# Kernel tuning notes

Hardware: AMD Instinct MI355X
Metric: run time of the kernel (lower is better)

Reference implementation:

```python
import jax, jax.numpy as jnp
import numpy as np

N, C_IN, C_OUT, K_CHEB, BATCH = 2048, 64, 64, 4, 8


def setup_inputs() -> dict:
    key = jax.random.key(0)
    k1, k2, k3, k4, k5 = jax.random.split(key, 5)
    # Xavier-uniform-like scales
    s_nn = float(np.sqrt(6.0 / (N + N)))
    s_th = float(np.sqrt(6.0 / (C_IN + C_OUT)))
    return {
        "X": jax.random.normal(k1, (BATCH, N, C_IN), dtype=jnp.float32),
        "Ws": jax.random.uniform(k2, (N, N), jnp.float32, -s_nn, s_nn),
        "W_alpha": jax.random.uniform(k3, (N, N), jnp.float32, -s_nn, s_nn),
        "Theta_s": jax.random.uniform(k4, (K_CHEB, C_IN, C_OUT), jnp.float32, -s_th, s_th),
        "Theta_d": jax.random.uniform(k5, (K_CHEB, C_IN, C_OUT), jnp.float32, -s_th, s_th),
    }


def reference(X, Ws, W_alpha, Theta_s, Theta_d):
    B, n, c_in = X.shape
    K = Theta_s.shape[0]

    # ---- static filter: sum_k (T_k(Ws) @ X) @ Theta_s[k] ----
    # T_0 = I, so T_0 @ X = X
    static_filter = jnp.einsum('bni,io->bno', X, Theta_s[0])
    if K > 1:
        T_prev2 = jnp.eye(n, dtype=X.dtype)
        T_prev1 = Ws  # T_1
        for k in range(1, K):
            TkX = jnp.einsum('nm,bmi->bni', T_prev1, X)
            static_filter = static_filter + jnp.einsum('bni,io->bno', TkX, Theta_s[k])
            if k + 1 < K:  # incremental Chebyshev recursion (same values as from-scratch)
                T_prev2, T_prev1 = T_prev1, 2.0 * (Ws @ T_prev1) - T_prev2

    # ---- dynamic filter ----
    # Wd = X @ (W_alpha @ X)^T  -> [B, n, n]
    WaX = jnp.einsum('nm,bmi->bni', W_alpha, X)
    Wd = jnp.einsum('bni,bmi->bnm', X, WaX)

    dynamic_filter = jnp.einsum('bni,io->bno', X, Theta_d[0])
    if K > 1:
        Td_prev2 = jnp.broadcast_to(jnp.eye(n, dtype=X.dtype), (B, n, n))
        Td_prev1 = Wd  # T_1
        for k in range(1, K):
            TkX = jnp.einsum('bnm,bmi->bni', Td_prev1, X)
            dynamic_filter = dynamic_filter + jnp.einsum('bni,io->bno', TkX, Theta_d[k])
            if k + 1 < K:
                Td_prev2, Td_prev1 = Td_prev1, 2.0 * jnp.matmul(Wd, Td_prev1) - Td_prev2

    return jax.nn.relu(static_filter) + jax.nn.relu(dynamic_filter)
```

## Files before the change

kernel.cpp:

```cpp
#include <hip/hip_runtime.h>

typedef __attribute__((ext_vector_type(8))) short bf16x8;
typedef __attribute__((ext_vector_type(4))) float f32x4;

__device__ __forceinline__ ushort f32_to_bf16(float f) {
    union { float f; unsigned u; } v; v.f = f;
    unsigned b = v.u + 0x7FFF + ((v.u >> 16) & 1);
    return (ushort)(b >> 16);
}
__device__ __forceinline__ float bf16_to_f32(ushort h) {
    union { unsigned u; float f; } v; v.u = ((unsigned)h) << 16;
    return v.f;
}
__device__ __forceinline__ void split2(float x, ushort& a, ushort& b) {
    a = f32_to_bf16(x); float r1 = x - bf16_to_f32(a);
    b = f32_to_bf16(r1);
}

__device__ __forceinline__ void vmwait8() { asm volatile("s_waitcnt vmcnt(8)" ::: "memory"); }
__device__ __forceinline__ void vmwait0() { asm volatile("s_waitcnt vmcnt(0)" ::: "memory"); }
__device__ __forceinline__ void lgwait0() { asm volatile("s_waitcnt lgkmcnt(0)" ::: "memory"); }
__device__ __forceinline__ void blockbar() {
    __builtin_amdgcn_sched_barrier(0);
    __builtin_amdgcn_s_barrier();
    __builtin_amdgcn_sched_barrier(0);
}

__device__ __forceinline__ void stage64x64(const ushort* gsrc, int row_stride_elems,
                                           char* lds, int t256) {
    const char* gb = (const char*)gsrc;
    const int rs = row_stride_elems * 2;
#pragma unroll
    for (int j = 0; j < 2; ++j) {
        int o = (j * 256 + t256) * 16;
        int row = o >> 7;
        int col = (o & 127) ^ ((row & 7) << 4);
        __builtin_amdgcn_global_load_lds(
            (const __attribute__((address_space(1))) unsigned int*)(gb + row * rs + col),
            (__attribute__((address_space(3))) unsigned int*)(lds + o), 16, 0, 0);
    }
}
__device__ __forceinline__ bf16x8 fragld(const char* lds, int row, int kbyte) {
    return *(const bf16x8*)(lds + (row << 7) + (kbyte ^ ((row & 7) << 4)));
}

__device__ __forceinline__ void stage64x128(const ushort* gsrc, char* lds, int t) {
    const char* gb = (const char*)gsrc;
#pragma unroll
    for (int j = 0; j < 4; ++j) {
        int o = (j * 256 + t) * 16;
        int row = o >> 8;
        int col = (o & 255) ^ ((row & 7) << 4);
        __builtin_amdgcn_global_load_lds(
            (const __attribute__((address_space(1))) unsigned int*)(gb + row * 4096 + col),
            (__attribute__((address_space(3))) unsigned int*)(lds + o), 16, 0, 0);
    }
}
__device__ __forceinline__ bf16x8 fragld256(const char* lds, int row, int kbyte) {
    return *(const bf16x8*)(lds + (row << 8) + (kbyte ^ ((row & 7) << 4)));
}

__global__ __launch_bounds__(256) void prep_all(const float* __restrict__ X,
        ushort* __restrict__ XT1, ushort* __restrict__ XT2,
        ushort* __restrict__ X1o, ushort* __restrict__ X2o,
        const float* __restrict__ Ws, ushort* __restrict__ Ws16,
        const float* __restrict__ Wa, ushort* __restrict__ Wa1,
        const float* __restrict__ Ths, ushort* __restrict__ ThsT) {
    __shared__ float tile[64][68];
    const int bx = blockIdx.x;
    const int t = threadIdx.x;
    if (bx < 256) {
        const int b = bx >> 5, n0 = (bx & 31) * 64;
#pragma unroll
        for (int it = 0; it < 4; ++it) {
            int f = it * 256 + t, r = f >> 4, q = (f & 15) * 4;
            float4 v = *(const float4*)&X[((size_t)b * 2048 + n0 + r) * 64 + q];
            tile[r][q + 0] = v.x; tile[r][q + 1] = v.y; tile[r][q + 2] = v.z; tile[r][q + 3] = v.w;
        }
        __syncthreads();
#pragma unroll
        for (int it = 0; it < 4; ++it) {
            int f = it * 256 + t, c = f >> 4, q = (f & 15) * 4;
            ushort4 h1, h2;
            split2(tile[q + 0][c], h1.x, h2.x); split2(tile[q + 1][c], h1.y, h2.y);
            split2(tile[q + 2][c], h1.z, h2.z); split2(tile[q + 3][c], h1.w, h2.w);
            size_t a = (size_t)(b * 64 + c) * 2048 + n0 + q;
            *(ushort4*)&XT1[a] = h1; *(ushort4*)&XT2[a] = h2;
        }
#pragma unroll
        for (int it = 0; it < 4; ++it) {
            int f = it * 256 + t, n = f >> 4, q = (f & 15) * 4;
            ushort4 h1, h2;
            split2(tile[n][q + 0], h1.x, h2.x); split2(tile[n][q + 1], h1.y, h2.y);
            split2(tile[n][q + 2], h1.z, h2.z); split2(tile[n][q + 3], h1.w, h2.w);
            size_t a = (size_t)(n0 + n) * 512 + b * 64 + q;
            *(ushort4*)&X1o[a] = h1; *(ushort4*)&X2o[a] = h2;
        }
    } else if (bx < 2304) {
        size_t idx = ((size_t)(bx - 256) * 256 + t) * 8;
#pragma unroll
        for (int h = 0; h < 2; ++h) {
            float4 v = *(const float4*)&Ws[idx + h * 4];
            ushort4 a;
            a.x = f32_to_bf16(v.x); a.y = f32_to_bf16(v.y);
            a.z = f32_to_bf16(v.z); a.w = f32_to_bf16(v.w);
            *(ushort4*)&Ws16[idx + h * 4] = a;
        }
    } else if (bx < 4352) {
        size_t idx = ((size_t)(bx - 2304) * 256 + t) * 8;
#pragma unroll
        for (int h = 0; h < 2; ++h) {
            float4 v = *(const float4*)&Wa[idx + h * 4];
            ushort4 a;
            a.x = f32_to_bf16(v.x); a.y = f32_to_bf16(v.y);
            a.z = f32_to_bf16(v.z); a.w = f32_to_bf16(v.w);
            *(ushort4*)&Wa1[idx + h * 4] = a;
        }
    } else {
        int idx = (bx - 4352) * 256 + t;
        int k = idx >> 12, o = (idx >> 6) & 63, i = idx & 63;
        ThsT[idx] = f32_to_bf16(Ths[k * 4096 + i * 64 + o]);
    }
}

template <int MODE>
__device__ __forceinline__ void gemm_sv2(int bx, const ushort* __restrict__ A,
        const ushort* __restrict__ BT, const ushort* __restrict__ CinT,
        ushort* __restrict__ YT, ushort* __restrict__ Yo, char* ls) {
    const int t = threadIdx.x;
    const int m0 = (bx & 31) * 64, c0 = (bx >> 5) * 64;
    const int w = t >> 6, lane = t & 63, l15 = lane & 15, l4 = lane >> 4;
    const int kb = w * 64 + l4 * 16;
    const ushort* Ap = A + (size_t)m0 * 2048;
    const ushort* Bp = BT + (size_t)c0 * 2048;

    f32x4 z = {0.f, 0.f, 0.f, 0.f};
    f32x4 acc[4][4];
#pragma unroll
    for (int i = 0; i < 4; ++i)
#pragma unroll
        for (int j = 0; j < 4; ++j) acc[i][j] = z;

    stage64x128(Ap, ls, t);
    stage64x128(Bp, ls + 16384, t);
    for (int ts = 0; ts < 16; ++ts) {
        char* cur = ls + (ts & 1) * 32768;
        if (ts < 15) {
            char* nxt = ls + ((ts + 1) & 1) * 32768;
            stage64x128(Ap + (ts + 1) * 128, nxt, t);
            stage64x128(Bp + (ts + 1) * 128, nxt + 16384, t);
            vmwait8();
        } else {
            vmwait0();
        }
        blockbar();
        bf16x8 aF[4], bF[4];
#pragma unroll
        for (int i = 0; i < 4; ++i) aF[i] = fragld256(cur, i * 16 + l15, kb);
#pragma unroll
        for (int j = 0; j < 4; ++j) bF[j] = fragld256(cur + 16384, j * 16 + l15, kb);
#pragma unroll
        for (int i = 0; i < 4; ++i)
#pragma unroll
            for (int j = 0; j < 4; ++j)
                acc[i][j] = __builtin_amdgcn_mfma_f32_16x16x32_bf16(aF[i], bF[j], acc[i][j], 0, 0, 0);
        lgwait0();
        blockbar();
    }

    float* red = (float*)ls;
    ushort* tileo = (ushort*)(ls + 50176);
    if (w < 3) {
#pragma unroll
        for (int i = 0; i < 4; ++i)
#pragma unroll
            for (int j = 0; j < 4; ++j) {
                const int row = i * 16 + l4 * 4;
                const int col = j * 16 + l15;
#pragma unroll
                for (int r = 0; r < 4; ++r) red[w * 4160 + (row + r) * 65 + col] = acc[i][j][r];
            }
    }
    __syncthreads();
    if (w == 3) {
#pragma unroll
        for (int i = 0; i < 4; ++i)
#pragma unroll
            for (int j = 0; j < 4; ++j) {
                const int row = i * 16 + l4 * 4;
                const int col = j * 16 + l15;
                float vv[4];
#pragma unroll
                for (int r = 0; r < 4; ++r) {
                    const int rr = (row + r) * 65 + col;
                    vv[r] = acc[i][j][r] + red[rr] + red[4160 + rr] + red[8320 + rr];
                }
                if (MODE == 1) {
                    ushort4 ci = *(const ushort4*)&CinT[(size_t)(c0 + col) * 2048 + m0 + row];
                    vv[0] = 2.f * vv[0] - bf16_to_f32(ci.x);
                    vv[1] = 2.f * vv[1] - bf16_to_f32(ci.y);
                    vv[2] = 2.f * vv[2] - bf16_to_f32(ci.z);
                    vv[3] = 2.f * vv[3] - bf16_to_f32(ci.w);
                }
                ushort4 p;
                p.x = f32_to_bf16(vv[0]); p.y = f32_to_bf16(vv[1]);
                p.z = f32_to_bf16(vv[2]); p.w = f32_to_bf16(vv[3]);
                *(ushort4*)&YT[(size_t)(c0 + col) * 2048 + m0 + row] = p;
                tileo[(row + 0) * 64 + col] = p.x;
                tileo[(row + 1) * 64 + col] = p.y;
                tileo[(row + 2) * 64 + col] = p.z;
                tileo[(row + 3) * 64 + col] = p.w;
            }
    }
    __syncthreads();
#pragma unroll
    for (int it = 0; it < 2; ++it) {
        int f = it * 256 + t;
        int row = f >> 3, ch = f & 7;
        *(uint4*)&Yo[(size_t)(m0 + row) * 512 + c0 + ch * 8] = *(uint4*)&tileo[row * 64 + ch * 8];
    }
}

__device__ __forceinline__ void gemm3v2(int bx, const ushort* __restrict__ A1,
        const ushort* __restrict__ B1, const ushort* __restrict__ B2,
        float* __restrict__ WaXT, char* ls) {
    const int t = threadIdx.x;
    const int m0 = (bx & 31) * 64, c0 = (bx >> 5) * 64;
    const int w = t >> 6, lane = t & 63, l15 = lane & 15, l4 = lane >> 4;
    const int kb = w * 64 + l4 * 16;

    f32x4 z = {0.f, 0.f, 0.f, 0.f};
    f32x4 acc[4][4];
#pragma unroll
    for (int i = 0; i < 4; ++i)
#pragma unroll
        for (int j = 0; j < 4; ++j) acc[i][j] = z;

    for (int k0 = 0; k0 < 2048; k0 += 128) {
        stage64x128(A1 + (size_t)m0 * 2048 + k0, ls, t);
        stage64x128(B1 + (size_t)c0 * 2048 + k0, ls + 16384, t);
        stage64x128(B2 + (size_t)c0 * 2048 + k0, ls + 32768, t);
        __syncthreads();
        bf16x8 aF[4], b1F[4], b2F[4];
#pragma unroll
        for (int i = 0; i < 4; ++i) {
            aF[i]  = fragld256(ls, i * 16 + l15, kb);
            b1F[i] = fragld256(ls + 16384, i * 16 + l15, kb);
            b2F[i] = fragld256(ls + 32768, i * 16 + l15, kb);
        }
#pragma unroll
        for (int i = 0; i < 4; ++i)
#pragma unroll
            for (int j = 0; j < 4; ++j) {
                f32x4 a = acc[i][j];
                a = __builtin_amdgcn_mfma_f32_16x16x32_bf16(aF[i], b1F[j], a, 0, 0, 0);
                a = __builtin_amdgcn_mfma_f32_16x16x32_bf16(aF[i], b2F[j], a, 0, 0, 0);
                acc[i][j] = a;
            }
        __syncthreads();
    }

    float* red = (float*)ls;
    if (w < 3) {
#pragma unroll
        for (int i = 0; i < 4; ++i)
#pragma unroll
            for (int j = 0; j < 4; ++j) {
                const int row = i * 16 + l4 * 4;
                const int col = j * 16 + l15;
#pragma unroll
                for (int r = 0; r < 4; ++r) red[w * 4160 + (row + r) * 65 + col] = acc[i][j][r];
            }
    }
    __syncthreads();
    if (w == 3) {
#pragma unroll
        for (int i = 0; i < 4; ++i)
#pragma unroll
            for (int j = 0; j < 4; ++j) {
                const int row = i * 16 + l4 * 4;
                const int col = j * 16 + l15;
                f32x4 v;
#pragma unroll
                for (int r = 0; r < 4; ++r) {
                    const int rr = (row + r) * 65 + col;
                    v[r] = acc[i][j][r] + red[rr] + red[4160 + rr] + red[8320 + rr];
                }
                *(f32x4*)&WaXT[(size_t)(c0 + col) * 2048 + m0 + row] = v;
            }
    }
}

__device__ __forceinline__ void gramv2(int bx, const float* __restrict__ WaXT,
        const ushort* __restrict__ XT1, const ushort* __restrict__ XT2,
        float* __restrict__ Gpart, char* lsraw) {
    const int b = bx & 7, chunk = bx >> 3;
    float (*Lw)[68] = (float(*)[68])lsraw;
    float (*Rx)[68] = (float(*)[68])(lsraw + 17408);
    const int t = threadIdx.x;
    const int n0 = chunk * 64;
    {
        const int r = t >> 2, q = (t & 3) * 16;
        size_t a = (size_t)(b * 64 + r) * 2048 + n0 + q;
#pragma unroll
        for (int h = 0; h < 4; ++h) {
            *(float4*)&Lw[r][q + h * 4] = *(const float4*)&WaXT[a + h * 4];
            ushort4 h1 = *(const ushort4*)&XT1[a + h * 4];
            ushort4 h2 = *(const ushort4*)&XT2[a + h * 4];
            Rx[r][q + h * 4 + 0] = bf16_to_f32(h1.x) + bf16_to_f32(h2.x);
            Rx[r][q + h * 4 + 1] = bf16_to_f32(h1.y) + bf16_to_f32(h2.y);
            Rx[r][q + h * 4 + 2] = bf16_to_f32(h1.z) + bf16_to_f32(h2.z);
            Rx[r][q + h * 4 + 3] = bf16_to_f32(h1.w) + bf16_to_f32(h2.w);
        }
    }
    __syncthreads();
    {
        const int tx = t & 15, ty = t >> 4;
        float acc[4][4] = {{0.f,0.f,0.f,0.f},{0.f,0.f,0.f,0.f},{0.f,0.f,0.f,0.f},{0.f,0.f,0.f,0.f}};
        for (int n = 0; n < 64; ++n) {
            float a[4], bb[4];
#pragma unroll
            for (int i = 0; i < 4; ++i) { a[i] = Lw[ty * 4 + i][n]; bb[i] = Rx[tx * 4 + i][n]; }
#pragma unroll
            for (int i = 0; i < 4; ++i)
#pragma unroll
                for (int j = 0; j < 4; ++j) acc[i][j] = fmaf(a[i], bb[j], acc[i][j]);
        }
        float* gp = Gpart + (size_t)(chunk * 8 + b) * 4096;
#pragma unroll
        for (int i = 0; i < 4; ++i)
            *(float4*)&gp[(ty * 4 + i) * 64 + tx * 4] =
                make_float4(acc[i][0], acc[i][1], acc[i][2], acc[i][3]);
    }
}

__device__ __forceinline__ void chebv2(int b, const float* __restrict__ Gpart,
        const float* __restrict__ Thd, ushort* __restrict__ DT1, ushort* __restrict__ DT2,
        char* lsraw) {
    float (*Gs)[68]  = (float(*)[68])lsraw;
    float (*C2s)[68] = (float(*)[68])(lsraw + 17408);
    float (*C3s)[68] = (float(*)[68])(lsraw + 34816);
    const int t = threadIdx.x;
    for (int i = t; i < 4096; i += 256) {
        float s = 0.f;
#pragma unroll
        for (int c = 0; c < 32; ++c) s += Gpart[((size_t)c * 8 + b) * 4096 + i];
        Gs[i >> 6][i & 63] = s;
    }
    __syncthreads();
    const int tx = t & 15, ty = t >> 4;
    const int r0 = ty * 4, c0 = tx * 4;

    {
        float p[4][4] = {{0,0,0,0},{0,0,0,0},{0,0,0,0},{0,0,0,0}};
        for (int k = 0; k < 64; ++k) {
            float ar[4] = {Gs[r0][k], Gs[r0+1][k], Gs[r0+2][k], Gs[r0+3][k]};
            float4 bv = *(const float4*)&Gs[k][c0];
            float br[4] = {bv.x, bv.y, bv.z, bv.w};
#pragma unroll
            for (int i = 0; i < 4; ++i)
#pragma unroll
                for (int j = 0; j < 4; ++j) p[i][j] = fmaf(ar[i], br[j], p[i][j]);
        }
#pragma unroll
        for (int i = 0; i < 4; ++i)
#pragma unroll
            for (int j = 0; j < 4; ++j)
                C2s[r0+i][c0+j] = 2.f * p[i][j] - ((r0+i) == (c0+j) ? 1.f : 0.f);
    }
    __syncthreads();
    {
        float q[4][4] = {{0,0,0,0},{0,0,0,0},{0,0,0,0},{0,0,0,0}};
        for (int k = 0; k < 64; ++k) {
            float ar[4] = {Gs[r0][k], Gs[r0+1][k], Gs[r0+2][k], Gs[r0+3][k]};
            float4 bv = *(const float4*)&C2s[k][c0];
            float br[4] = {bv.x, bv.y, bv.z, bv.w};
#pragma unroll
            for (int i = 0; i < 4; ++i)
#pragma unroll
                for (int j = 0; j < 4; ++j) q[i][j] = fmaf(ar[i], br[j], q[i][j]);
        }
#pragma unroll
        for (int i = 0; i < 4; ++i)
#pragma unroll
            for (int j = 0; j < 4; ++j)
                C3s[r0+i][c0+j] = 2.f * q[i][j] - Gs[r0+i][c0+j];
    }
    __syncthreads();
    float d[4][4];
    {
#pragma unroll
        for (int i = 0; i < 4; ++i) {
            float4 t0 = *(const float4*)&Thd[(r0+i) * 64 + c0];
            d[i][0] = t0.x; d[i][1] = t0.y; d[i][2] = t0.z; d[i][3] = t0.w;
        }
        for (int k = 0; k < 64; ++k) {
            float4 t1 = *(const float4*)&Thd[4096 + k * 64 + c0];
            float4 t2 = *(const float4*)&Thd[8192 + k * 64 + c0];
            float4 t3 = *(const float4*)&Thd[12288 + k * 64 + c0];
            float a1[4] = {Gs[r0][k], Gs[r0+1][k], Gs[r0+2][k], Gs[r0+3][k]};
            float a2[4] = {C2s[r0][k], C2s[r0+1][k], C2s[r0+2][k], C2s[r0+3][k]};
            float a3[4] = {C3s[r0][k], C3s[r0+1][k], C3s[r0+2][k], C3s[r0+3][k]};
            float b1[4] = {t1.x, t1.y, t1.z, t1.w};
            float b2[4] = {t2.x, t2.y, t2.z, t2.w};
            float b3[4] = {t3.x, t3.y, t3.z, t3.w};
#pragma unroll
            for (int i = 0; i < 4; ++i)
#pragma unroll
                for (int j = 0; j < 4; ++j) {
                    d[i][j] = fmaf(a1[i], b1[j], d[i][j]);
                    d[i][j] = fmaf(a2[i], b2[j], d[i][j]);
                    d[i][j] = fmaf(a3[i], b3[j], d[i][j]);
                }
        }
    }
    __syncthreads();
#pragma unroll
    for (int i = 0; i < 4; ++i)
#pragma unroll
        for (int j = 0; j < 4; ++j) Gs[r0 + i][c0 + j] = d[i][j];
    __syncthreads();
#pragma unroll
    for (int it = 0; it < 16; ++it) {
        int idx = it * 256 + t;
        int o = idx >> 6, ii = idx & 63;
        ushort h1, h2;
        split2(Gs[ii][o], h1, h2);
        DT1[b * 4096 + idx] = h1;
        DT2[b * 4096 + idx] = h2;
    }
}

__global__ __launch_bounds__(256, 2) void mega1(const ushort* __restrict__ Wa1,
        const ushort* __restrict__ XT1, const ushort* __restrict__ XT2,
        float* __restrict__ WaXT,
        const ushort* __restrict__ Ws16, ushort* __restrict__ Y1T, ushort* __restrict__ Y1o) {
    __shared__ __align__(16) char ls[65536];
    const int bx = blockIdx.x;
    if (bx < 256) gemm3v2(bx, Wa1, XT1, XT2, WaXT, ls);
    else          gemm_sv2<0>(bx - 256, Ws16, XT1, nullptr, Y1T, Y1o, ls);
}

__global__ __launch_bounds__(256, 2) void mega2(const ushort* __restrict__ Ws16,
        const ushort* __restrict__ Y1T, const ushort* __restrict__ XT1,
        ushort* __restrict__ Y2T, ushort* __restrict__ Y2o,
        const float* __restrict__ WaXT, const ushort* __restrict__ XT2,
        float* __restrict__ Gpart) {
    __shared__ __align__(16) char ls[65536];
    const int bx = blockIdx.x;
    if (bx < 256) gemm_sv2<1>(bx, Ws16, Y1T, XT1, Y2T, Y2o, ls);
    else          gramv2(bx - 256, WaXT, XT1, XT2, Gpart, ls);
}

__global__ __launch_bounds__(256, 2) void mega3(const ushort* __restrict__ Ws16,
        const ushort* __restrict__ Y2T, const ushort* __restrict__ Y1T,
        ushort* __restrict__ Y3T, ushort* __restrict__ Y3o,
        const float* __restrict__ Gpart, const float* __restrict__ Thd,
        ushort* __restrict__ DT1, ushort* __restrict__ DT2) {
    __shared__ __align__(16) char ls[65536];
    const int bx = blockIdx.x;
    if (bx < 256) gemm_sv2<1>(bx, Ws16, Y2T, Y1T, Y3T, Y3o, ls);
    else          chebv2(bx - 256, Gpart, Thd, DT1, DT2, ls);
}

__global__ __launch_bounds__(256) void ep_fused(const ushort* __restrict__ ThsT,
                                                const ushort* __restrict__ DT1, const ushort* __restrict__ DT2,
                                                const ushort* __restrict__ X1o, const ushort* __restrict__ X2o,
                                                const ushort* __restrict__ Y1o, const ushort* __restrict__ Y2o,
                                                const ushort* __restrict__ Y3o,
                                                float* __restrict__ out) {
    __shared__ __align__(16) char ls[65536];
    const int b = blockIdx.y, n0 = blockIdx.x * 64;
    const int t = threadIdx.x, lane = t & 63, w = t >> 6, wr = w >> 1, wc = w & 1;
    const int l15 = lane & 15, l4 = lane >> 4;
    stage64x64(X1o + (size_t)n0 * 512 + b * 64, 512, ls + 0 * 8192, t);
    stage64x64(Y1o + (size_t)n0 * 512 + b * 64, 512, ls + 1 * 8192, t);
    stage64x64(Y2o + (size_t)n0 * 512 + b * 64, 512, ls + 2 * 8192, t);
    stage64x64(Y3o + (size_t)n0 * 512 + b * 64, 512, ls + 3 * 8192, t);
    stage64x64(ThsT + 0 * 4096, 64, ls + 4 * 8192, t);
    stage64x64(ThsT + 1 * 4096, 64, ls + 5 * 8192, t);
    stage64x64(ThsT + 2 * 4096, 64, ls + 6 * 8192, t);
    stage64x64(ThsT + 3 * 4096, 64, ls + 7 * 8192, t);
    __syncthreads();
    f32x4 z = {0.f, 0.f, 0.f, 0.f};
    f32x4 as[2][2], ad[2][2];
    as[0][0] = z; as[0][1] = z; as[1][0] = z; as[1][1] = z;
    ad[0][0] = z; ad[0][1] = z; ad[1][0] = z; ad[1][1] = z;
#pragma unroll
    for (int s = 0; s < 2; ++s) {
        const int kb = s * 64 + l4 * 16;
#pragma unroll
        for (int p = 0; p < 4; ++p) {
            bf16x8 aF[2], bF[2];
#pragma unroll
            for (int f = 0; f < 2; ++f) {
                aF[f] = fragld(ls + (4 + p) * 8192, wr * 32 + f * 16 + l15, kb);
                bF[f] = fragld(ls + p * 8192, wc * 32 + f * 16 + l15, kb);
            }
#pragma unroll
            for (int i = 0; i < 2; ++i)
#pragma unroll
                for (int j = 0; j < 2; ++j)
                    as[i][j] = __builtin_amdgcn_mfma_f32_16x16x32_bf16(aF[i], bF[j], as[i][j], 0, 0, 0);
        }
    }
    __syncthreads();
    stage64x64(DT1 + b * 4096, 64, ls + 1 * 8192, t);
    stage64x64(DT2 + b * 4096, 64, ls + 2 * 8192, t);
    stage64x64(X2o + (size_t)n0 * 512 + b * 64, 512, ls + 3 * 8192, t);
    __syncthreads();
#pragma unroll
    for (int s = 0; s < 2; ++s) {
        const int kb = s * 64 + l4 * 16;
        bf16x8 a1[2], a2[2], b0[2], b3[2];
#pragma unroll
        for (int f = 0; f < 2; ++f) {
            a1[f] = fragld(ls + 1 * 8192, wr * 32 + f * 16 + l15, kb);
            a2[f] = fragld(ls + 2 * 8192, wr * 32 + f * 16 + l15, kb);
            b0[f] = fragld(ls + 0 * 8192, wc * 32 + f * 16 + l15, kb);
            b3[f] = fragld(ls + 3 * 8192, wc * 32 + f * 16 + l15, kb);
        }
#pragma unroll
        for (int i = 0; i < 2; ++i)
#pragma unroll
            for (int j = 0; j < 2; ++j) {
                f32x4 a = ad[i][j];
                a = __builtin_amdgcn_mfma_f32_16x16x32_bf16(a1[i], b0[j], a, 0, 0, 0);
                a = __builtin_amdgcn_mfma_f32_16x16x32_bf16(a1[i], b3[j], a, 0, 0, 0);
                a = __builtin_amdgcn_mfma_f32_16x16x32_bf16(a2[i], b0[j], a, 0, 0, 0);
                ad[i][j] = a;
            }
    }
#pragma unroll
    for (int i = 0; i < 2; ++i)
#pragma unroll
        for (int j = 0; j < 2; ++j) {
            const int ob = wr * 32 + i * 16 + l4 * 4;
            const int nn = wc * 32 + j * 16 + l15;
            float4 o4;
            o4.x = fmaxf(as[i][j][0], 0.f) + fmaxf(ad[i][j][0], 0.f);
            o4.y = fmaxf(as[i][j][1], 0.f) + fmaxf(ad[i][j][1], 0.f);
            o4.z = fmaxf(as[i][j][2], 0.f) + fmaxf(ad[i][j][2], 0.f);
            o4.w = fmaxf(as[i][j][3], 0.f) + fmaxf(ad[i][j][3], 0.f);
            *(float4*)&out[((size_t)b * 2048 + n0 + nn) * 64 + ob] = o4;
        }
}

extern "C" void kernel_launch(void* const* d_in, const int* in_sizes, int n_in,
                              void* d_out, int out_size, void* d_ws, size_t ws_size,
                              hipStream_t stream) {
    (void)in_sizes; (void)n_in; (void)out_size;
    const float* X   = (const float*)d_in[0];
    const float* Ws  = (const float*)d_in[1];
    const float* Wa  = (const float*)d_in[2];
    const float* Ths = (const float*)d_in[3];
    const float* Thd = (const float*)d_in[4];

    char* p = (char*)d_ws;
    auto alloc = [&](size_t bytes) { char* r = p; p += (bytes + 255) & ~(size_t)255; return r; };
    ushort* XT1 = (ushort*)alloc(512ull * 2048 * 2);
    ushort* XT2 = (ushort*)alloc(512ull * 2048 * 2);
    ushort* X1o = (ushort*)alloc(2048ull * 512 * 2);
    ushort* X2o = (ushort*)alloc(2048ull * 512 * 2);
    ushort* Ws16 = (ushort*)alloc(2048ull * 2048 * 2);
    ushort* Wa1 = (ushort*)alloc(2048ull * 2048 * 2);
    ushort* Y1T = (ushort*)alloc(512ull * 2048 * 2);
    ushort* Y2T = (ushort*)alloc(512ull * 2048 * 2);
    ushort* Y3T = (ushort*)alloc(512ull * 2048 * 2);
    ushort* Y1o = (ushort*)alloc(2048ull * 512 * 2);
    ushort* Y2o = (ushort*)alloc(2048ull * 512 * 2);
    ushort* Y3o = (ushort*)alloc(2048ull * 512 * 2);
    float*  Gpart = (float*)alloc(32ull * 8 * 4096 * 4);
    ushort* DT1 = (ushort*)alloc(8ull * 4096 * 2);
    ushort* DT2 = (ushort*)alloc(8ull * 4096 * 2);
    ushort* ThsT = (ushort*)alloc(4ull * 4096 * 2);
    if ((size_t)(p - (char*)d_ws) > ws_size) return;
    float* WaXT = (float*)d_out;

    prep_all<<<4416, 256, 0, stream>>>(X, XT1, XT2, X1o, X2o, Ws, Ws16, Wa, Wa1, Ths, ThsT);
    mega1<<<512, 256, 0, stream>>>(Wa1, XT1, XT2, WaXT, Ws16, Y1T, Y1o);
    mega2<<<512, 256, 0, stream>>>(Ws16, Y1T, XT1, Y2T, Y2o, WaXT, XT2, Gpart);
    mega3<<<264, 256, 0, stream>>>(Ws16, Y2T, Y1T, Y3T, Y3o, Gpart, Thd, DT1, DT2);
    ep_fused<<<dim3(32, 8), 256, 0, stream>>>(ThsT, DT1, DT2, X1o, X2o, Y1o, Y2o, Y3o, (float*)d_out);
}
```

Before: 87.85 us.

## Double mega-kernel block size to eight waves splitting output columns

The three fused GEMM mega-kernels now launch 512 threads per block instead of 256. Each GEMM wave covers half of the 64-column output tile and one of four K slices. This halves per-wave accumulator registers and doubles the waves available to hide latency. The cross-wave reduction, the LDS staging loops and the gram/cheb helper bodies are reworked for the larger block, with idle threads masked where needed. In exchange, A fragments are loaded redundantly from LDS by both column waves, and launch_bounds(512,4) may cap registers tightly enough to cause spills.

```diff
diff --git a/kernel.cpp b/kernel.cpp
--- a/kernel.cpp
+++ b/kernel.cpp
@@ -17,7 +17,7 @@
     b = f32_to_bf16(r1);
 }
 
-__device__ __forceinline__ void vmwait8() { asm volatile("s_waitcnt vmcnt(8)" ::: "memory"); }
+__device__ __forceinline__ void vmwait4() { asm volatile("s_waitcnt vmcnt(4)" ::: "memory"); }
 __device__ __forceinline__ void vmwait0() { asm volatile("s_waitcnt vmcnt(0)" ::: "memory"); }
 __device__ __forceinline__ void lgwait0() { asm volatile("s_waitcnt lgkmcnt(0)" ::: "memory"); }
 __device__ __forceinline__ void blockbar() {
@@ -44,11 +44,11 @@
     return *(const bf16x8*)(lds + (row << 7) + (kbyte ^ ((row & 7) << 4)));
 }
 
-__device__ __forceinline__ void stage64x128(const ushort* gsrc, char* lds, int t) {
+__device__ __forceinline__ void stage64x128_512(const ushort* gsrc, char* lds, int t) {
     const char* gb = (const char*)gsrc;
 #pragma unroll
-    for (int j = 0; j < 4; ++j) {
-        int o = (j * 256 + t) * 16;
+    for (int j = 0; j < 2; ++j) {
+        int o = (j * 512 + t) * 16;
         int row = o >> 8;
         int col = (o & 255) ^ ((row & 7) << 4);
         __builtin_amdgcn_global_load_lds(
@@ -124,76 +124,78 @@
 }
 
 template <int MODE>
-__device__ __forceinline__ void gemm_sv2(int bx, const ushort* __restrict__ A,
+__device__ __forceinline__ void gemm_sv3(int bx, const ushort* __restrict__ A,
         const ushort* __restrict__ BT, const ushort* __restrict__ CinT,
         ushort* __restrict__ YT, ushort* __restrict__ Yo, char* ls) {
     const int t = threadIdx.x;
     const int m0 = (bx & 31) * 64, c0 = (bx >> 5) * 64;
-    const int w = t >> 6, lane = t & 63, l15 = lane & 15, l4 = lane >> 4;
-    const int kb = w * 64 + l4 * 16;
+    const int w = t >> 6, kw = w >> 1, nw = w & 1;
+    const int lane = t & 63, l15 = lane & 15, l4 = lane >> 4;
+    const int kb = kw * 64 + l4 * 16;
     const ushort* Ap = A + (size_t)m0 * 2048;
     const ushort* Bp = BT + (size_t)c0 * 2048;
 
     f32x4 z = {0.f, 0.f, 0.f, 0.f};
-    f32x4 acc[4][4];
-#pragma unroll
-    for (int i = 0; i < 4; ++i)
-#pragma unroll
-        for (int j = 0; j < 4; ++j) acc[i][j] = z;
-
-    stage64x128(Ap, ls, t);
-    stage64x128(Bp, ls + 16384, t);
+    f32x4 acc[4][2];
+#pragma unroll
+    for (int i = 0; i < 4; ++i) { acc[i][0] = z; acc[i][1] = z; }
+
+    stage64x128_512(Ap, ls, t);
+    stage64x128_512(Bp, ls + 16384, t);
     for (int ts = 0; ts < 16; ++ts) {
         char* cur = ls + (ts & 1) * 32768;
         if (ts < 15) {
             char* nxt = ls + ((ts + 1) & 1) * 32768;
-            stage64x128(Ap + (ts + 1) * 128, nxt, t);
-            stage64x128(Bp + (ts + 1) * 128, nxt + 16384, t);
-            vmwait8();
+            stage64x128_512(Ap + (ts + 1) * 128, nxt, t);
+            stage64x128_512(Bp + (ts + 1) * 128, nxt + 16384, t);
+            vmwait4();
         } else {
             vmwait0();
         }
         blockbar();
-        bf16x8 aF[4], bF[4];
+        bf16x8 aF[4], bF[2];
 #pragma unroll
         for (int i = 0; i < 4; ++i) aF[i] = fragld256(cur, i * 16 + l15, kb);
 #pragma unroll
-        for (int j = 0; j < 4; ++j) bF[j] = fragld256(cur + 16384, j * 16 + l15, kb);
-#pragma unroll
-        for (int i = 0; i < 4; ++i)
-#pragma unroll
-            for (int j = 0; j < 4; ++j)
+        for (int j = 0; j < 2; ++j) bF[j] = fragld256(cur + 16384, nw * 32 + j * 16 + l15, kb);
+#pragma unroll
+        for (int i = 0; i < 4; ++i)
+#pragma unroll
+            for (int j = 0; j < 2; ++j)
                 acc[i][j] = __builtin_amdgcn_mfma_f32_16x16x32_bf16(aF[i], bF[j], acc[i][j], 0, 0, 0);
         lgwait0();
         blockbar();
     }
 
     float* red = (float*)ls;
-    ushort* tileo = (ushort*)(ls + 50176);
-    if (w < 3) {
-#pragma unroll
-        for (int i = 0; i < 4; ++i)
-#pragma unroll
-            for (int j = 0; j < 4; ++j) {
+    ushort* tileo = (ushort*)(ls + 51200);
+    if (kw > 0) {
+        float* rg = red + ((kw - 1) * 2 + nw) * 2112;
+#pragma unroll
+        for (int i = 0; i < 4; ++i)
+#pragma unroll
+            for (int j = 0; j < 2; ++j) {
                 const int row = i * 16 + l4 * 4;
-                const int col = j * 16 + l15;
-#pragma unroll
-                for (int r = 0; r < 4; ++r) red[w * 4160 + (row + r) * 65 + col] = acc[i][j][r];
-            }
-    }
-    __syncthreads();
-    if (w == 3) {
-#pragma unroll
-        for (int i = 0; i < 4; ++i)
-#pragma unroll
-            for (int j = 0; j < 4; ++j) {
+                const int colL = j * 16 + l15;
+#pragma unroll
+                for (int r = 0; r < 4; ++r) rg[(row + r) * 33 + colL] = acc[i][j][r];
+            }
+    }
+    __syncthreads();
+    if (kw == 0) {
+#pragma unroll
+        for (int i = 0; i < 4; ++i)
+#pragma unroll
+            for (int j = 0; j < 2; ++j) {
                 const int row = i * 16 + l4 * 4;
-                const int col = j * 16 + l15;
+                const int colL = j * 16 + l15;
+                const int col = nw * 32 + colL;
                 float vv[4];
 #pragma unroll
                 for (int r = 0; r < 4; ++r) {
-                    const int rr = (row + r) * 65 + col;
-                    vv[r] = acc[i][j][r] + red[rr] + red[4160 + rr] + red[8320 + rr];
+                    const int rr = (row + r) * 33 + colL;
+                    vv[r] = acc[i][j][r] + red[nw * 2112 + rr]
+                          + red[(2 + nw) * 2112 + rr] + red[(4 + nw) * 2112 + rr];
                 }
                 if (MODE == 1) {
                     ushort4 ci = *(const ushort4*)&CinT[(size_t)(c0 + col) * 2048 + m0 + row];
@@ -213,45 +215,43 @@
             }
     }
     __syncthreads();
-#pragma unroll
-    for (int it = 0; it < 2; ++it) {
-        int f = it * 256 + t;
-        int row = f >> 3, ch = f & 7;
+    {
+        int row = t >> 3, ch = t & 7;
         *(uint4*)&Yo[(size_t)(m0 + row) * 512 + c0 + ch * 8] = *(uint4*)&tileo[row * 64 + ch * 8];
     }
 }
 
-__device__ __forceinline__ void gemm3v2(int bx, const ushort* __restrict__ A1,
+__device__ __forceinline__ void gemm3v3(int bx, const ushort* __restrict__ A1,
         const ushort* __restrict__ B1, const ushort* __restrict__ B2,
         float* __restrict__ WaXT, char* ls) {
     const int t = threadIdx.x;
     const int m0 = (bx & 31) * 64, c0 = (bx >> 5) * 64;
-    const int w = t >> 6, lane = t & 63, l15 = lane & 15, l4 = lane >> 4;
-    const int kb = w * 64 + l4 * 16;
+    const int w = t >> 6, kw = w >> 1, nw = w & 1;
+    const int lane = t & 63, l15 = lane & 15, l4 = lane >> 4;
+    const int kb = kw * 64 + l4 * 16;
 
     f32x4 z = {0.f, 0.f, 0.f, 0.f};
-    f32x4 acc[4][4];
-#pragma unroll
-    for (int i = 0; i < 4; ++i)
-#pragma unroll
-        for (int j = 0; j < 4; ++j) acc[i][j] = z;
+    f32x4 acc[4][2];
+#pragma unroll
+    for (int i = 0; i < 4; ++i) { acc[i][0] = z; acc[i][1] = z; }
 
     for (int k0 = 0; k0 < 2048; k0 += 128) {
-        stage64x128(A1 + (size_t)m0 * 2048 + k0, ls, t);
-        stage64x128(B1 + (size_t)c0 * 2048 + k0, ls + 16384, t);
-        stage64x128(B2 + (size_t)c0 * 2048 + k0, ls + 32768, t);
+        stage64x128_512(A1 + (size_t)m0 * 2048 + k0, ls, t);
+        stage64x128_512(B1 + (size_t)c0 * 2048 + k0, ls + 16384, t);
+        stage64x128_512(B2 + (size_t)c0 * 2048 + k0, ls + 32768, t);
         __syncthreads();
-        bf16x8 aF[4], b1F[4], b2F[4];
-#pragma unroll
-        for (int i = 0; i < 4; ++i) {
-            aF[i]  = fragld256(ls, i * 16 + l15, kb);
-            b1F[i] = fragld256(ls + 16384, i * 16 + l15, kb);
-            b2F[i] = fragld256(ls + 32768, i * 16 + l15, kb);
-        }
-#pragma unroll
-        for (int i = 0; i < 4; ++i)
-#pragma unroll
-            for (int j = 0; j < 4; ++j) {
+        bf16x8 aF[4], b1F[2], b2F[2];
+#pragma unroll
+        for (int i = 0; i < 4; ++i) aF[i] = fragld256(ls, i * 16 + l15, kb);
+#pragma unroll
+        for (int j = 0; j < 2; ++j) {
+            b1F[j] = fragld256(ls + 16384, nw * 32 + j * 16 + l15, kb);
+            b2F[j] = fragld256(ls + 32768, nw * 32 + j * 16 + l15, kb);
+        }
+#pragma unroll
+        for (int i = 0; i < 4; ++i)
+#pragma unroll
+            for (int j = 0; j < 2; ++j) {
                 f32x4 a = acc[i][j];
                 a = __builtin_amdgcn_mfma_f32_16x16x32_bf16(aF[i], b1F[j], a, 0, 0, 0);
                 a = __builtin_amdgcn_mfma_f32_16x16x32_bf16(aF[i], b2F[j], a, 0, 0, 0);
@@ -261,50 +261,54 @@
     }
 
     float* red = (float*)ls;
-    if (w < 3) {
-#pragma unroll
-        for (int i = 0; i < 4; ++i)
-#pragma unroll
-            for (int j = 0; j < 4; ++j) {
+    if (kw > 0) {
+        float* rg = red + ((kw - 1) * 2 + nw) * 2112;
+#pragma unroll
+        for (int i = 0; i < 4; ++i)
+#pragma unroll
+            for (int j = 0; j < 2; ++j) {
                 const int row = i * 16 + l4 * 4;
-                const int col = j * 16 + l15;
-#pragma unroll
-                for (int r = 0; r < 4; ++r) red[w * 4160 + (row + r) * 65 + col] = acc[i][j][r];
-            }
-    }
-    __syncthreads();
-    if (w == 3) {
-#pragma unroll
-        for (int i = 0; i < 4; ++i)
-#pragma unroll
-            for (int j = 0; j < 4; ++j) {
+                const int colL = j * 16 + l15;
+#pragma unroll
+                for (int r = 0; r < 4; ++r) rg[(row + r) * 33 + colL] = acc[i][j][r];
+            }
+    }
+    __syncthreads();
+    if (kw == 0) {
+#pragma unroll
+        for (int i = 0; i < 4; ++i)
+#pragma unroll
+            for (int j = 0; j < 2; ++j) {
                 const int row = i * 16 + l4 * 4;
-                const int col = j * 16 + l15;
+                const int colL = j * 16 + l15;
+                const int col = nw * 32 + colL;
                 f32x4 v;
 #pragma unroll
                 for (int r = 0; r < 4; ++r) {
-                    const int rr = (row + r) * 65 + col;
-                    v[r] = acc[i][j][r] + red[rr] + red[4160 + rr] + red[8320 + rr];
+                    const int rr = (row + r) * 33 + colL;
+                    v[r] = acc[i][j][r] + red[nw * 2112 + rr]
+                         + red[(2 + nw) * 2112 + rr] + red[(4 + nw) * 2112 + rr];
                 }
                 *(f32x4*)&WaXT[(size_t)(c0 + col) * 2048 + m0 + row] = v;
             }
     }
 }
 
-__device__ __forceinline__ void gramv2(int bx, const float* __restrict__ WaXT,
+__device__ __forceinline__ void gram_body(int bx, const float* __restrict__ WaXT,
         const ushort* __restrict__ XT1, const ushort* __restrict__ XT2,
         float* __restrict__ Gpart, char* lsraw) {
     const int b = bx & 7, chunk = bx >> 3;
     float (*Lw)[68] = (float(*)[68])lsraw;
-    float (*Rx)[68] = (float(*)[68])(lsraw + 17408);
+    float (*Rx)[68] = (float(*)[68])(lsraw + 64 * 68 * 4);
     const int t = threadIdx.x;
     const int n0 = chunk * 64;
     {
-        const int r = t >> 2, q = (t & 3) * 16;
+        const int r = t >> 3, q = (t & 7) * 8;
         size_t a = (size_t)(b * 64 + r) * 2048 + n0 + q;
-#pragma unroll
-        for (int h = 0; h < 4; ++h) {
-            *(float4*)&Lw[r][q + h * 4] = *(const float4*)&WaXT[a + h * 4];
+        *(float4*)&Lw[r][q]     = *(const float4*)&WaXT[a];
+        *(float4*)&Lw[r][q + 4] = *(const float4*)&WaXT[a + 4];
+#pragma unroll
+        for (int h = 0; h < 2; ++h) {
             ushort4 h1 = *(const ushort4*)&XT1[a + h * 4];
             ushort4 h2 = *(const ushort4*)&XT2[a + h * 4];
             Rx[r][q + h * 4 + 0] = bf16_to_f32(h1.x) + bf16_to_f32(h2.x);
@@ -314,7 +318,7 @@
         }
     }
     __syncthreads();
-    {
+    if (t < 256) {
         const int tx = t & 15, ty = t >> 4;
         float acc[4][4] = {{0.f,0.f,0.f,0.f},{0.f,0.f,0.f,0.f},{0.f,0.f,0.f,0.f},{0.f,0.f,0.f,0.f}};
         for (int n = 0; n < 64; ++n) {
@@ -334,24 +338,25 @@
     }
 }
 
-__device__ __forceinline__ void chebv2(int b, const float* __restrict__ Gpart,
+__device__ __forceinline__ void cheb_body(int b, const float* __restrict__ Gpart,
         const float* __restrict__ Thd, ushort* __restrict__ DT1, ushort* __restrict__ DT2,
         char* lsraw) {
     float (*Gs)[68]  = (float(*)[68])lsraw;
     float (*C2s)[68] = (float(*)[68])(lsraw + 17408);
     float (*C3s)[68] = (float(*)[68])(lsraw + 34816);
     const int t = threadIdx.x;
-    for (int i = t; i < 4096; i += 256) {
+    for (int i = t; i < 4096; i += 512) {
         float s = 0.f;
 #pragma unroll
         for (int c = 0; c < 32; ++c) s += Gpart[((size_t)c * 8 + b) * 4096 + i];
         Gs[i >> 6][i & 63] = s;
     }
     __syncthreads();
-    const int tx = t & 15, ty = t >> 4;
+    const int tx = t & 15, ty = (t >> 4) & 15;
     const int r0 = ty * 4, c0 = tx * 4;
-
-    {
+    const bool act = t < 256;
+
+    if (act) {
         float p[4][4] = {{0,0,0,0},{0,0,0,0},{0,0,0,0},{0,0,0,0}};
         for (int k = 0; k < 64; ++k) {
             float ar[4] = {Gs[r0][k], Gs[r0+1][k], Gs[r0+2][k], Gs[r0+3][k]};
@@ -369,7 +374,7 @@
                 C2s[r0+i][c0+j] = 2.f * p[i][j] - ((r0+i) == (c0+j) ? 1.f : 0.f);
     }
     __syncthreads();
-    {
+    if (act) {
         float q[4][4] = {{0,0,0,0},{0,0,0,0},{0,0,0,0},{0,0,0,0}};
         for (int k = 0; k < 64; ++k) {
             float ar[4] = {Gs[r0][k], Gs[r0+1][k], Gs[r0+2][k], Gs[r0+3][k]};
@@ -388,7 +393,7 @@
     }
     __syncthreads();
     float d[4][4];
-    {
+    if (act) {
 #pragma unroll
         for (int i = 0; i < 4; ++i) {
             float4 t0 = *(const float4*)&Thd[(r0+i) * 64 + c0];
@@ -415,14 +420,15 @@
         }
     }
     __syncthreads();
-#pragma unroll
-    for (int i = 0; i < 4; ++i)
-#pragma unroll
-        for (int j = 0; j < 4; ++j) Gs[r0 + i][c0 + j] = d[i][j];
-    __syncthreads();
-#pragma unroll
-    for (int it = 0; it < 16; ++it) {
-        int idx = it * 256 + t;
+    if (act) {
+#pragma unroll
+        for (int i = 0; i < 4; ++i)
+#pragma unroll
+            for (int j = 0; j < 4; ++j) Gs[r0 + i][c0 + j] = d[i][j];
+    }
+    __syncthreads();
+    for (int it = 0; it < 8; ++it) {
+        int idx = it * 512 + t;
         int o = idx >> 6, ii = idx & 63;
         ushort h1, h2;
         split2(Gs[ii][o], h1, h2);
@@ -431,36 +437,36 @@
     }
 }
 
-__global__ __launch_bounds__(256, 2) void mega1(const ushort* __restrict__ Wa1,
+__global__ __launch_bounds__(512, 4) void mega1(const ushort* __restrict__ Wa1,
         const ushort* __restrict__ XT1, const ushort* __restrict__ XT2,
         float* __restrict__ WaXT,
         const ushort* __restrict__ Ws16, ushort* __restrict__ Y1T, ushort* __restrict__ Y1o) {
     __shared__ __align__(16) char ls[65536];
     const int bx = blockIdx.x;
-    if (bx < 256) gemm3v2(bx, Wa1, XT1, XT2, WaXT, ls);
-    else          gemm_sv2<0>(bx - 256, Ws16, XT1, nullptr, Y1T, Y1o, ls);
-}
-
-__global__ __launch_bounds__(256, 2) void mega2(const ushort* __restrict__ Ws16,
+    if (bx < 256) gemm3v3(bx, Wa1, XT1, XT2, WaXT, ls);
+    else          gemm_sv3<0>(bx - 256, Ws16, XT1, nullptr, Y1T, Y1o, ls);
+}
+
+__global__ __launch_bounds__(512, 4) void mega2(const ushort* __restrict__ Ws16,
         const ushort* __restrict__ Y1T, const ushort* __restrict__ XT1,
         ushort* __restrict__ Y2T, ushort* __restrict__ Y2o,
         const float* __restrict__ WaXT, const ushort* __restrict__ XT2,
         float* __restrict__ Gpart) {
     __shared__ __align__(16) char ls[65536];
     const int bx = blockIdx.x;
-    if (bx < 256) gemm_sv2<1>(bx, Ws16, Y1T, XT1, Y2T, Y2o, ls);
-    else          gramv2(bx - 256, WaXT, XT1, XT2, Gpart, ls);
-}
-
-__global__ __launch_bounds__(256, 2) void mega3(const ushort* __restrict__ Ws16,
+    if (bx < 256) gemm_sv3<1>(bx, Ws16, Y1T, XT1, Y2T, Y2o, ls);
+    else          gram_body(bx - 256, WaXT, XT1, XT2, Gpart, ls);
+}
+
+__global__ __launch_bounds__(512, 4) void mega3(const ushort* __restrict__ Ws16,
         const ushort* __restrict__ Y2T, const ushort* __restrict__ Y1T,
         ushort* __restrict__ Y3T, ushort* __restrict__ Y3o,
         const float* __restrict__ Gpart, const float* __restrict__ Thd,
         ushort* __restrict__ DT1, ushort* __restrict__ DT2) {
     __shared__ __align__(16) char ls[65536];
     const int bx = blockIdx.x;
-    if (bx < 256) gemm_sv2<1>(bx, Ws16, Y2T, Y1T, Y3T, Y3o, ls);
-    else          chebv2(bx - 256, Gpart, Thd, DT1, DT2, ls);
+    if (bx < 256) gemm_sv3<1>(bx, Ws16, Y2T, Y1T, Y3T, Y3o, ls);
+    else          cheb_body(bx - 256, Gpart, Thd, DT1, DT2, ls);
 }
 
 __global__ __launch_bounds__(256) void ep_fused(const ushort* __restrict__ ThsT,
@@ -578,8 +584,8 @@
     float* WaXT = (float*)d_out;
 
     prep_all<<<4416, 256, 0, stream>>>(X, XT1, XT2, X1o, X2o, Ws, Ws16, Wa, Wa1, Ths, ThsT);
-    mega1<<<512, 256, 0, stream>>>(Wa1, XT1, XT2, WaXT, Ws16, Y1T, Y1o);
-    mega2<<<512, 256, 0, stream>>>(Ws16, Y1T, XT1, Y2T, Y2o, WaXT, XT2, Gpart);
-    mega3<<<264, 256, 0, stream>>>(Ws16, Y2T, Y1T, Y3T, Y3o, Gpart, Thd, DT1, DT2);
+    mega1<<<512, 512, 0, stream>>>(Wa1, XT1, XT2, WaXT, Ws16, Y1T, Y1o);
+    mega2<<<512, 512, 0, stream>>>(Ws16, Y1T, XT1, Y2T, Y2o, WaXT, XT2, Gpart);
+    mega3<<<264, 512, 0, stream>>>(Ws16, Y2T, Y1T, Y3T, Y3o, Gpart, Thd, DT1, DT2);
     ep_fused<<<dim3(32, 8), 256, 0, stream>>>(ThsT, DT1, DT2, X1o, X2o, Y1o, Y2o, Y3o, (float*)d_out);
 }
```

New measurement: 86.80 us. No clear change (-1.2%).
